# Kernel tuning notes

Hardware: AMD Instinct MI355X
Metric: run time of the kernel (lower is better)

## Reference

```python
import jax, jax.numpy as jnp
import numpy as np

R = 4                      # search_range
D = 2 * R + 1              # 9 -> 81 cost channels
FILTERS = [128, 128, 96, 64, 32, 2]


def mish(x):
    return x * jnp.tanh(jax.nn.softplus(x))


def sep_conv(x, dw, pw, b, act):
    # depthwise 3x3 (depth_multiplier=1), then pointwise 1x1, bias after pointwise
    y = jax.lax.conv_general_dilated(
        x, dw, window_strides=(1, 1), padding='SAME',
        dimension_numbers=('NHWC', 'HWIO', 'NHWC'),
        feature_group_count=x.shape[-1])
    y = jax.lax.conv_general_dilated(
        y, pw, window_strides=(1, 1), padding='SAME',
        dimension_numbers=('NHWC', 'HWIO', 'NHWC'))
    if b is not None:
        y = y + b
    return mish(y) if act else y


def cost_volume(prv, nxt):
    B, H, W, C = prv.shape
    pad = jnp.pad(nxt, ((0, 0), (R, R), (R, R), (0, 0)))
    # (2R+1)^2 shifted correlations, mean over channels (matches tf.reduce_mean axis=3)
    costs = [jnp.mean(prv * pad[:, i:i + H, j:j + W, :], axis=3)
             for i in range(D) for j in range(D)]
    return jnp.stack(costs, axis=3)  # [B,H,W,81]


def setup_inputs() -> dict:
    key = jax.random.key(0)
    ks = jax.random.split(key, 40)
    B, H, W, C = 8, 128, 128, 128
    inp = {
        'prv': jax.random.normal(ks[0], (B, H, W, C), jnp.float32),
        'nxt': jax.random.normal(ks[1], (B, H, W, C), jnp.float32),
    }
    in_ch = [D * D + 2 * C] + FILTERS[:-1]  # [337,128,128,96,64,32]
    ki = 2
    for i, (ci, f) in enumerate(zip(in_ch, FILTERS)):
        inp[f'dw{i}'] = jax.random.normal(ks[ki], (3, 3, 1, ci), jnp.float32) * 0.05; ki += 1
        inp[f'pw{i}'] = jax.random.normal(ks[ki], (1, 1, ci, f), jnp.float32) * 0.05; ki += 1
        if i < len(FILTERS) - 1:  # last layer: use_bias=False
            inp[f'b{i}'] = jnp.zeros((f,), jnp.float32)
    return inp


def reference(prv, nxt,
              dw0, pw0, b0, dw1, pw1, b1, dw2, pw2, b2,
              dw3, pw3, b3, dw4, pw4, b4, dw5, pw5):
    cost = cost_volume(prv, nxt)
    x = jnp.concatenate([cost, prv, nxt], axis=-1)
    x = sep_conv(x, dw0, pw0, b0, True)
    x = sep_conv(x, dw1, pw1, b1, True)
    x = sep_conv(x, dw2, pw2, b2, True)
    x = sep_conv(x, dw3, pw3, b3, True)
    x = sep_conv(x, dw4, pw4, b4, True)
    x = sep_conv(x, dw5, pw5, None, False)  # flow head: no bias, no activation
    return x
```

## Files before the change

kernel.cpp:

```cpp
#include <hip/hip_runtime.h>
#include <math.h>

#define BATCH 8
#define HH 128
#define WW 128
#define CC 128
#define RR 4
#define DDIM 9
#define NS 81
#define NSP 96
#define HWPIX (HH*WW)
#define DSLAB 1032

typedef short  short8  __attribute__((ext_vector_type(8)));
typedef float  f32x4   __attribute__((ext_vector_type(4)));

__device__ __forceinline__ short bf16h(float f){
    unsigned u = __float_as_uint(f);
    u += 0x7fffu + ((u >> 16) & 1u);
    return (short)(u >> 16);
}
__device__ __forceinline__ float bf16f(short s){
    return __uint_as_float(((unsigned)(unsigned short)s) << 16);
}
__device__ __forceinline__ float mish_f(float x){
    float xc = fminf(x, 30.f);
    float t = expf(xc);
    float u = t*t + 2.f*t;
    return x * (u / (u + 2.f));
}

__device__ __forceinline__ void gld16(float* lds, const float* g){
    __builtin_amdgcn_global_load_lds(
        (const __attribute__((address_space(1))) unsigned int*)g,
        (__attribute__((address_space(3))) unsigned int*)lds, 16, 0, 0);
}

__device__ __forceinline__ void lds_barrier(){
    __asm volatile("s_waitcnt lgkmcnt(0)\n\ts_barrier" ::: "memory");
}

__global__ void zero_k(float* p, int n){
    int i = blockIdx.x*256 + threadIdx.x;
    if(i < n) p[i] = 0.f;
}

__global__ __launch_bounds__(256,2) void cost_kernel(
    const float* __restrict__ prv, const float* __restrict__ nxt,
    const float* __restrict__ zb, float* __restrict__ cost)
{
    __shared__ float nx[2][2304*2];
    const int tid = threadIdx.x;
    const int tx = tid & 15, ty = tid >> 4;
    const int x0 = blockIdx.x*16, y0 = blockIdx.y*16, b = blockIdx.z;

    float acc[NS];
#pragma unroll
    for(int s=0;s<NS;s++) acc[s]=0.f;

    const float* prvp = prv + (((size_t)b*HH + (y0+ty))*WW + (x0+tx))*CC;
    const float* nxb  = nxt + (size_t)b*HH*WW*CC;

    auto stagec = [&](int c0, int pb){
        float* xp = &nx[pb][0];
#pragma unroll
        for(int it=0;it<5;it++){
            int e = it*256 + tid;
            if(e < 1152){
                int q = (e >= 576) ? 1 : 0;
                int p = e - q*576;
                int row = p/24, col = p - row*24;
                int hy = y0 - RR + row, hx = x0 - RR + col;
                bool ok = hy>=0 && hy<HH && hx>=0 && hx<WW;
                const float* gp = ok ? (nxb + ((size_t)hy*WW + hx)*CC + c0 + q*4)
                                     : zb;
                gld16(xp + e*4, gp);
            }
        }
    };

    float4 pAr = *(const float4*)(prvp);
    float4 pBr = *(const float4*)(prvp + 4);
    stagec(0, 0);
    int pb = 0;
    for(int c0=0;c0<CC;c0+=8){
        __syncthreads();
        float4 A = pAr, Bv = pBr;
        if(c0+8 < CC){
            pAr = *(const float4*)(prvp + c0 + 8);
            pBr = *(const float4*)(prvp + c0 + 12);
            stagec(c0+8, pb^1);
        }
        const float* xp = &nx[pb][0];
#pragma unroll
        for(int i=0;i<DDIM;i++){
            const float* rp = xp + (((ty+i)*24 + tx))*4;
#pragma unroll
            for(int j=0;j<DDIM;j++){
                float4 n0 = *(const float4*)(rp + j*4);
                float4 n1 = *(const float4*)(rp + j*4 + 2304);
                float s = acc[i*DDIM+j];
                s = fmaf(A.x,n0.x,s);  s = fmaf(A.y,n0.y,s);
                s = fmaf(A.z,n0.z,s);  s = fmaf(A.w,n0.w,s);
                s = fmaf(Bv.x,n1.x,s); s = fmaf(Bv.y,n1.y,s);
                s = fmaf(Bv.z,n1.z,s); s = fmaf(Bv.w,n1.w,s);
                acc[i*DDIM+j] = s;
            }
        }
        pb ^= 1;
    }
    float* op = cost + (((size_t)b*HH + (y0+ty))*WW + (x0+tx))*NSP;
#pragma unroll
    for(int g=0; g<NSP/4; g++){
        float4 v;
        int s = g*4;
        v.x = (s   < NS) ? acc[s  ]*(1.f/128.f) : 0.f;
        v.y = (s+1 < NS) ? acc[s+1]*(1.f/128.f) : 0.f;
        v.z = (s+2 < NS) ? acc[s+2]*(1.f/128.f) : 0.f;
        v.w = (s+3 < NS) ? acc[s+3]*(1.f/128.f) : 0.f;
        *(float4*)(op + s) = v;
    }
}

__global__ void prep_pw(const float* __restrict__ src, short* __restrict__ dh,
                        short* __restrict__ dl, int K, int N, int NP, int total,
                        int remap)
{
    int idx = blockIdx.x*256 + threadIdx.x;
    if(idx >= total) return;
    int j  = idx & 7;
    int n  = (idx>>3) % NP;
    int k8 = (idx>>3) / NP;
    int k  = k8*8 + j;
    if(remap) k = (k < 81) ? k : ((k < 96) ? -1 : k - 15);
    float v = (k>=0 && k<K && n<N) ? src[(size_t)k*N + n] : 0.f;
    short h = bf16h(v);
    dh[idx] = h;
    dl[idx] = bf16h(v - bf16f(h));
}

__global__ void prep_dw(const float* __restrict__ src, float* __restrict__ dst,
                        int K, int K0, int remap, int total)
{
    int idx = blockIdx.x*256 + threadIdx.x;
    if(idx >= total) return;
    int k = idx / K0, c = idx - k*K0;
    int cr = c;
    if(remap) cr = (c < 81) ? c : ((c < 96) ? -1 : c - 15);
    dst[idx] = (cr>=0 && cr<K) ? src[k*K + cr] : 0.f;
}

template<int CINR,int K0,int COUT,int NP,bool BIAS,bool ACT,bool CONCAT>
__global__ __launch_bounds__(256,2) void sep_mfma(
    const float* __restrict__ xin, const float* __restrict__ cost,
    const float* __restrict__ prv, const float* __restrict__ nxt,
    const float* __restrict__ dwp, const short* __restrict__ wh,
    const short* __restrict__ wl, const float* __restrict__ bias,
    const float* __restrict__ zb, float* __restrict__ out)
{
    constexpr int TN = NP/32;
    __shared__ float xs[2][180*36];
    __shared__ short dshh[4*DSLAB];
    __shared__ short dshl[4*DSLAB];
    __shared__ float dwls[2][9*32];

    const int tid = threadIdx.x;
    const int x0 = blockIdx.x*16, y0 = blockIdx.y*8, b = blockIdx.z;
    const int lane = tid & 63;
    const int wv   = tid >> 6;
    const int wm   = wv >> 1, wn = wv & 1;
    const int l15  = lane & 15, quad = lane >> 4;

    f32x4 acc[4][TN];
#pragma unroll
    for(int i=0;i<4;i++)
#pragma unroll
        for(int nt=0;nt<TN;nt++) acc[i][nt] = (f32x4){0.f,0.f,0.f,0.f};

    auto stage = [&](int c0, int pb){
        if(tid < 72)
            gld16(&dwls[pb][(tid>>3)*32 + (tid&7)*4],
                  dwp + (tid>>3)*K0 + c0 + (tid&7)*4);
        const float* src; int str, coff;
        if(CONCAT){
            if(c0 < 96)      { src = cost; str = NSP; coff = c0; }
            else if(c0 < 224){ src = prv;  str = 128; coff = c0-96; }
            else             { src = nxt;  str = 128; coff = c0-224; }
        } else { src = xin; str = CINR; coff = c0; }
        const float* sb = src + (size_t)b*HH*WW*str + coff;
        float* xp = &xs[pb][0];
#pragma unroll
        for(int it=0;it<7;it++){
            int e = it*256 + tid;
            if(e < 1620){
                int hp = e/9, q = e - hp*9;
                int hy = y0-1 + hp/18, hx = x0-1 + hp%18;
                bool ok = (q < 8) && hy>=0 && hy<HH && hx>=0 && hx<WW;
                const float* gp = ok ? (sb + ((size_t)hy*WW + hx)*str + q*4)
                                     : zb;
                gld16(xp + hp*36 + q*4, gp);
            }
        }
    };

    const int c4  = tid & 7;
    const int pxg = tid >> 3;
    const int dpy = pxg >> 2;
    const int dxb = (pxg & 3) * 4;

    stage(0, 0);
    int pb = 0;
    for(int c0=0;c0<K0;c0+=32){
        __syncthreads();
        const int k8 = (c0>>3) + quad;
        short8 Bh[TN], Bl[TN];
#pragma unroll
        for(int nt=0;nt<TN;nt++){
            int n = wn*(NP/2) + nt*16 + l15;
            size_t off = ((size_t)k8*NP + n)*8;
            Bh[nt] = *(const short8*)(wh + off);
            Bl[nt] = *(const short8*)(wl + off);
        }
        if(c0+32 < K0) stage(c0+32, pb^1);
        const float* xp = &xs[pb][0];
        const float* dwc = &dwls[pb][0];
        {
            float4 o[4];
#pragma unroll
            for(int dx=0;dx<4;dx++) o[dx] = make_float4(0.f,0.f,0.f,0.f);
#pragma unroll
            for(int kh=0;kh<3;kh++){
                float4 xw[6];
#pragma unroll
                for(int t=0;t<6;t++)
                    xw[t] = *(const float4*)&xp[((dpy+kh)*18 + dxb + t)*36 + c4*4];
#pragma unroll
                for(int kw=0;kw<3;kw++){
                    float4 w4 = *(const float4*)&dwc[(kh*3+kw)*32 + c4*4];
#pragma unroll
                    for(int dx=0;dx<4;dx++){
                        float4 xv = xw[kw+dx];
                        o[dx].x = fmaf(xv.x,w4.x,o[dx].x);
                        o[dx].y = fmaf(xv.y,w4.y,o[dx].y);
                        o[dx].z = fmaf(xv.z,w4.z,o[dx].z);
                        o[dx].w = fmaf(xv.w,w4.w,o[dx].w);
                    }
                }
            }
            const int wbase = (c4>>1)*DSLAB + (pxg*4)*8 + (c4&1)*4;
#pragma unroll
            for(int dx=0;dx<4;dx++){
                float4 s = o[dx];
                short h0=bf16h(s.x), h1=bf16h(s.y), h2=bf16h(s.z), h3=bf16h(s.w);
                short l0=bf16h(s.x-bf16f(h0)), l1=bf16h(s.y-bf16f(h1));
                short l2=bf16h(s.z-bf16f(h2)), l3=bf16h(s.w-bf16f(h3));
                *(short4*)&dshh[wbase + dx*8] = make_short4(h0,h1,h2,h3);
                *(short4*)&dshl[wbase + dx*8] = make_short4(l0,l1,l2,l3);
            }
        }
        lds_barrier();
#pragma unroll
        for(int i=0;i<4;i++){
            int ab = quad*DSLAB + (wm*64 + i*16 + l15)*8;
            short8 Ah = *(const short8*)&dshh[ab];
            short8 Al = *(const short8*)&dshl[ab];
#pragma unroll
            for(int nt=0;nt<TN;nt++){
                f32x4 c = acc[i][nt];
                c = __builtin_amdgcn_mfma_f32_16x16x32_bf16(Ah,Bh[nt],c,0,0,0);
                c = __builtin_amdgcn_mfma_f32_16x16x32_bf16(Al,Bh[nt],c,0,0,0);
                c = __builtin_amdgcn_mfma_f32_16x16x32_bf16(Ah,Bl[nt],c,0,0,0);
                acc[i][nt] = c;
            }
        }
        lds_barrier();
        pb ^= 1;
    }
#pragma unroll
    for(int i=0;i<4;i++){
        int pxb = wm*64 + i*16 + quad*4;
#pragma unroll
        for(int nt=0;nt<TN;nt++){
            int cout = wn*(NP/2) + nt*16 + l15;
            if(cout < COUT){
                float bv = BIAS ? bias[cout] : 0.f;
#pragma unroll
                for(int r=0;r<4;r++){
                    int p = pxb + r;
                    int y = y0 + (p>>4), x = x0 + (p&15);
                    float v = acc[i][nt][r] + bv;
                    if(ACT) v = mish_f(v);
                    out[(((size_t)b*HH + y)*WW + x)*COUT + cout] = v;
                }
            }
        }
    }
}

extern "C" void kernel_launch(void* const* d_in, const int* in_sizes, int n_in,
                              void* d_out, int out_size, void* d_ws, size_t ws_size,
                              hipStream_t stream)
{
    (void)in_sizes; (void)n_in; (void)out_size;
    const float* prv = (const float*)d_in[0];
    const float* nxt = (const float*)d_in[1];
    const float* dws[6] = {(const float*)d_in[2],(const float*)d_in[5],(const float*)d_in[8],
                           (const float*)d_in[11],(const float*)d_in[14],(const float*)d_in[17]};
    const float* pws[6] = {(const float*)d_in[3],(const float*)d_in[6],(const float*)d_in[9],
                           (const float*)d_in[12],(const float*)d_in[15],(const float*)d_in[18]};
    const float* b0  = (const float*)d_in[4];
    const float* b1  = (const float*)d_in[7];
    const float* b2  = (const float*)d_in[10];
    const float* b3  = (const float*)d_in[13];
    const float* b4  = (const float*)d_in[16];

    const int   Ks[6]   = {337,128,128, 96, 64, 32};
    const int   K0s[6]  = {352,128,128, 96, 64, 32};
    const int   Ns[6]   = {128,128, 96, 64, 32,  2};
    const int   NPs[6]  = {128,128, 96, 64, 32, 32};
    const int   rmp[6]  = {  1,  0,  0,  0,  0,  0};
    size_t offs[6]; size_t E = 0;
    for(int i=0;i<6;i++){ offs[i] = E; E += (size_t)K0s[i]*NPs[i]; }
    size_t dwoffs[6]; size_t Edw = 0;
    for(int i=0;i<6;i++){ dwoffs[i] = Edw; Edw += (size_t)9*K0s[i]; }

    short* Whs = (short*)d_ws;
    short* Wls = Whs + E;
    float* Dwp = (float*)((char*)d_ws + ((E*2*sizeof(short) + 255) & ~(size_t)255));
    float* Zb  = Dwp + Edw;
    size_t wbytes = (((char*)(Zb + 64) - (char*)d_ws) + 255) & ~(size_t)255;

    zero_k<<<1,64,0,stream>>>(Zb, 64);
    for(int i=0;i<6;i++){
        int total = K0s[i]*NPs[i];
        prep_pw<<<(total+255)/256,256,0,stream>>>(pws[i], Whs+offs[i], Wls+offs[i],
                                                  Ks[i], Ns[i], NPs[i], total, rmp[i]);
        int tdw = 9*K0s[i];
        prep_dw<<<(tdw+255)/256,256,0,stream>>>(dws[i], Dwp+dwoffs[i],
                                                Ks[i], K0s[i], rmp[i], tdw);
    }

    const size_t per_batch_floats = (size_t)HWPIX * (NSP + 128 + 128);
    size_t avail = (ws_size > wbytes) ? (ws_size - wbytes) : 0;
    int NB = (int)(avail / (per_batch_floats * sizeof(float)));
    if(NB > BATCH) NB = BATCH;
    if(NB < 1)     NB = 1;
    while(BATCH % NB) NB--;

    float* fbase = (float*)((char*)d_ws + wbytes);
    float* costb = fbase;
    float* bufA  = costb + (size_t)NB*HWPIX*NSP;
    float* bufB  = bufA  + (size_t)NB*HWPIX*128;

    for(int bb=0; bb<BATCH; bb+=NB){
        const float* prv_o = prv + (size_t)bb*HWPIX*CC;
        const float* nxt_o = nxt + (size_t)bb*HWPIX*CC;
        float*       out_o = (float*)d_out + (size_t)bb*HWPIX*2;
        dim3 gc(WW/16, HH/16, NB);
        dim3 gs(WW/16, HH/8,  NB);

        cost_kernel<<<gc,256,0,stream>>>(prv_o, nxt_o, Zb, costb);
        sep_mfma<337,352,128,128,true ,true ,true ><<<gs,256,0,stream>>>(nullptr, costb, prv_o, nxt_o, Dwp+dwoffs[0], Whs+offs[0], Wls+offs[0], b0, Zb, bufA);
        sep_mfma<128,128,128,128,true ,true ,false><<<gs,256,0,stream>>>(bufA, nullptr,nullptr,nullptr, Dwp+dwoffs[1], Whs+offs[1], Wls+offs[1], b1, Zb, bufB);
        sep_mfma<128,128, 96, 96,true ,true ,false><<<gs,256,0,stream>>>(bufB, nullptr,nullptr,nullptr, Dwp+dwoffs[2], Whs+offs[2], Wls+offs[2], b2, Zb, bufA);
        sep_mfma< 96, 96, 64, 64,true ,true ,false><<<gs,256,0,stream>>>(bufA, nullptr,nullptr,nullptr, Dwp+dwoffs[3], Whs+offs[3], Wls+offs[3], b3, Zb, bufB);
        sep_mfma< 64, 64, 32, 32,true ,true ,false><<<gs,256,0,stream>>>(bufB, nullptr,nullptr,nullptr, Dwp+dwoffs[4], Whs+offs[4], Wls+offs[4], b4, Zb, bufA);
        sep_mfma< 32, 32,  2, 32,false,false,false><<<gs,256,0,stream>>>(bufA, nullptr,nullptr,nullptr, Dwp+dwoffs[5], Whs+offs[5], Wls+offs[5], nullptr, Zb, out_o);
    }
}
```

Measured before the change: 576.9 us.

## Compute cost volume with split-bf16 MFMA instead of scalar FMAs

Replaces the scalar-FMA correlation kernel with an MFMA kernel. Each wave computes 16x16 pixel-by-shift tiles per row offset, using a hi/lo bf16 split (four MFMAs per tile) to keep roughly fp32 accuracy. Shifted nxt tiles are converted to bf16 hi/lo in LDS with register-prefetch double staging, and only the valid diagonal band of each tile is written out. This wastes part of each MFMA on shifts outside the band and adds conversion work in exchange for matrix-core throughput.

```diff
diff --git a/kernel.cpp b/kernel.cpp
--- a/kernel.cpp
+++ b/kernel.cpp
@@ -45,80 +45,135 @@
     if(i < n) p[i] = 0.f;
 }
 
-__global__ __launch_bounds__(256,2) void cost_kernel(
+__device__ __forceinline__ void cvt8(const float4& a, const float4& b,
+                                     short8& h, short8& l){
+    float v0=a.x,v1=a.y,v2=a.z,v3=a.w,v4=b.x,v5=b.y,v6=b.z,v7=b.w;
+    short h0=bf16h(v0),h1=bf16h(v1),h2=bf16h(v2),h3=bf16h(v3);
+    short h4=bf16h(v4),h5=bf16h(v5),h6=bf16h(v6),h7=bf16h(v7);
+    h[0]=h0;h[1]=h1;h[2]=h2;h[3]=h3;h[4]=h4;h[5]=h5;h[6]=h6;h[7]=h7;
+    l[0]=bf16h(v0-bf16f(h0)); l[1]=bf16h(v1-bf16f(h1));
+    l[2]=bf16h(v2-bf16f(h2)); l[3]=bf16h(v3-bf16f(h3));
+    l[4]=bf16h(v4-bf16f(h4)); l[5]=bf16h(v5-bf16f(h5));
+    l[6]=bf16h(v6-bf16f(h6)); l[7]=bf16h(v7-bf16f(h7));
+}
+
+__global__ __launch_bounds__(512,4) void cost_mfma(
     const float* __restrict__ prv, const float* __restrict__ nxt,
-    const float* __restrict__ zb, float* __restrict__ cost)
+    float* __restrict__ cost)
 {
-    __shared__ float nx[2][2304*2];
-    const int tid = threadIdx.x;
-    const int tx = tid & 15, ty = tid >> 4;
+    __shared__ short bhs[24*4*24*8];
+    __shared__ short bls[24*4*24*8];
+    const int tid  = threadIdx.x;
+    const int lane = tid & 63, wv = tid >> 6;
+    const int l15  = lane & 15, quad = lane >> 4;
     const int x0 = blockIdx.x*16, y0 = blockIdx.y*16, b = blockIdx.z;
-
-    float acc[NS];
-#pragma unroll
-    for(int s=0;s<NS;s++) acc[s]=0.f;
-
-    const float* prvp = prv + (((size_t)b*HH + (y0+ty))*WW + (x0+tx))*CC;
+    const int Y = wv*2;
+
+    const float* prvb = prv + (((size_t)b*HH + y0)*WW + x0)*CC;
     const float* nxb  = nxt + (size_t)b*HH*WW*CC;
 
-    auto stagec = [&](int c0, int pb){
-        float* xp = &nx[pb][0];
-#pragma unroll
-        for(int it=0;it<5;it++){
-            int e = it*256 + tid;
-            if(e < 1152){
-                int q = (e >= 576) ? 1 : 0;
-                int p = e - q*576;
-                int row = p/24, col = p - row*24;
-                int hy = y0 - RR + row, hx = x0 - RR + col;
-                bool ok = hy>=0 && hy<HH && hx>=0 && hx<WW;
-                const float* gp = ok ? (nxb + ((size_t)hy*WW + hx)*CC + c0 + q*4)
-                                     : zb;
-                gld16(xp + e*4, gp);
-            }
+    f32x4 acc[2][9][2];
+#pragma unroll
+    for(int yy=0;yy<2;yy++)
+#pragma unroll
+        for(int i=0;i<9;i++){
+            acc[yy][i][0] = (f32x4){0.f,0.f,0.f,0.f};
+            acc[yy][i][1] = (f32x4){0.f,0.f,0.f,0.f};
+        }
+
+    if(tid < 256){
+        float* zp = cost + (((size_t)b*HH + y0 + (tid>>4))*WW + x0 + (tid&15))*NSP;
+        zp[81]=0.f; zp[82]=0.f; zp[83]=0.f;
+        float4 z4 = make_float4(0.f,0.f,0.f,0.f);
+        *(float4*)(zp+84)=z4; *(float4*)(zp+88)=z4; *(float4*)(zp+92)=z4;
+    }
+
+    float4 sreg[9];
+    auto sload = [&](int kc){
+#pragma unroll
+        for(int s=0;s<9;s++){
+            int e = s*512 + tid;
+            int px = e >> 3, q = e & 7;
+            int r = px/24, c = px - r*24;
+            int hy = y0 - 4 + r, hx = x0 - 4 + c;
+            bool ok = hy>=0 && hy<HH && hx>=0 && hx<WW;
+            sreg[s] = ok ? *(const float4*)(nxb + ((size_t)hy*WW + hx)*CC + kc*32 + q*4)
+                         : make_float4(0.f,0.f,0.f,0.f);
         }
     };
-
-    float4 pAr = *(const float4*)(prvp);
-    float4 pBr = *(const float4*)(prvp + 4);
-    stagec(0, 0);
-    int pb = 0;
-    for(int c0=0;c0<CC;c0+=8){
+    sload(0);
+
+    for(int kc=0; kc<4; kc++){
         __syncthreads();
-        float4 A = pAr, Bv = pBr;
-        if(c0+8 < CC){
-            pAr = *(const float4*)(prvp + c0 + 8);
-            pBr = *(const float4*)(prvp + c0 + 12);
-            stagec(c0+8, pb^1);
-        }
-        const float* xp = &nx[pb][0];
-#pragma unroll
-        for(int i=0;i<DDIM;i++){
-            const float* rp = xp + (((ty+i)*24 + tx))*4;
-#pragma unroll
-            for(int j=0;j<DDIM;j++){
-                float4 n0 = *(const float4*)(rp + j*4);
-                float4 n1 = *(const float4*)(rp + j*4 + 2304);
-                float s = acc[i*DDIM+j];
-                s = fmaf(A.x,n0.x,s);  s = fmaf(A.y,n0.y,s);
-                s = fmaf(A.z,n0.z,s);  s = fmaf(A.w,n0.w,s);
-                s = fmaf(Bv.x,n1.x,s); s = fmaf(Bv.y,n1.y,s);
-                s = fmaf(Bv.z,n1.z,s); s = fmaf(Bv.w,n1.w,s);
-                acc[i*DDIM+j] = s;
-            }
-        }
-        pb ^= 1;
-    }
-    float* op = cost + (((size_t)b*HH + (y0+ty))*WW + (x0+tx))*NSP;
-#pragma unroll
-    for(int g=0; g<NSP/4; g++){
-        float4 v;
-        int s = g*4;
-        v.x = (s   < NS) ? acc[s  ]*(1.f/128.f) : 0.f;
-        v.y = (s+1 < NS) ? acc[s+1]*(1.f/128.f) : 0.f;
-        v.z = (s+2 < NS) ? acc[s+2]*(1.f/128.f) : 0.f;
-        v.w = (s+3 < NS) ? acc[s+3]*(1.f/128.f) : 0.f;
-        *(float4*)(op + s) = v;
+#pragma unroll
+        for(int s=0;s<9;s++){
+            int e = s*512 + tid;
+            int px = e >> 3, q = e & 7;
+            int r = px/24, c = px - r*24;
+            int base = ((r*4 + (q>>1))*24 + c)*8 + (q&1)*4;
+            float4 v = sreg[s];
+            short h0=bf16h(v.x), h1=bf16h(v.y), h2=bf16h(v.z), h3=bf16h(v.w);
+            *(short4*)&bhs[base] = make_short4(h0,h1,h2,h3);
+            *(short4*)&bls[base] = make_short4(bf16h(v.x-bf16f(h0)),
+                                               bf16h(v.y-bf16f(h1)),
+                                               bf16h(v.z-bf16f(h2)),
+                                               bf16h(v.w-bf16f(h3)));
+        }
+        if(kc < 3) sload(kc+1);
+        short8 Ah[2], Al[2];
+#pragma unroll
+        for(int yy=0; yy<2; yy++){
+            const float* ap = prvb + ((size_t)(Y+yy)*WW + l15)*CC + kc*32 + quad*8;
+            float4 f0v = *(const float4*)ap;
+            float4 f1v = *(const float4*)(ap+4);
+            cvt8(f0v, f1v, Ah[yy], Al[yy]);
+        }
+        lds_barrier();
+#pragma unroll
+        for(int rr=0; rr<10; rr++){
+            int r  = Y + rr;
+            int rb = (r*4 + quad)*24*8;
+            short8 Bh0 = *(const short8*)&bhs[rb + l15*8];
+            short8 Bl0 = *(const short8*)&bls[rb + l15*8];
+            short8 Bh1 = *(const short8*)&bhs[rb + (8+l15)*8];
+            short8 Bl1 = *(const short8*)&bls[rb + (8+l15)*8];
+#pragma unroll
+            for(int yy=0; yy<2; yy++){
+                int i = rr - yy;
+                if(i >= 0 && i <= 8){
+                    f32x4 c0 = acc[yy][i][0];
+                    c0 = __builtin_amdgcn_mfma_f32_16x16x32_bf16(Ah[yy],Bh0,c0,0,0,0);
+                    c0 = __builtin_amdgcn_mfma_f32_16x16x32_bf16(Al[yy],Bh0,c0,0,0,0);
+                    c0 = __builtin_amdgcn_mfma_f32_16x16x32_bf16(Ah[yy],Bl0,c0,0,0,0);
+                    c0 = __builtin_amdgcn_mfma_f32_16x16x32_bf16(Al[yy],Bl0,c0,0,0,0);
+                    acc[yy][i][0] = c0;
+                    f32x4 c1 = acc[yy][i][1];
+                    c1 = __builtin_amdgcn_mfma_f32_16x16x32_bf16(Ah[yy],Bh1,c1,0,0,0);
+                    c1 = __builtin_amdgcn_mfma_f32_16x16x32_bf16(Al[yy],Bh1,c1,0,0,0);
+                    c1 = __builtin_amdgcn_mfma_f32_16x16x32_bf16(Ah[yy],Bl1,c1,0,0,0);
+                    c1 = __builtin_amdgcn_mfma_f32_16x16x32_bf16(Al[yy],Bl1,c1,0,0,0);
+                    acc[yy][i][1] = c1;
+                }
+            }
+        }
+    }
+    const float sc = 1.f/128.f;
+#pragma unroll
+    for(int yy=0; yy<2; yy++){
+        float* orow = cost + (((size_t)b*HH + (y0+Y+yy))*WW + x0)*NSP;
+#pragma unroll
+        for(int i=0;i<9;i++){
+#pragma unroll
+            for(int rg=0; rg<4; rg++){
+                int m  = quad*4 + rg;
+                int j0 = l15 - m;
+                if(j0 >= 0 && j0 <= 8)
+                    orow[(size_t)m*NSP + i*9 + j0] = acc[yy][i][0][rg]*sc;
+                int j1 = 8 + l15 - m;
+                if(l15 >= 8 && j1 <= 8)
+                    orow[(size_t)m*NSP + i*9 + j1] = acc[yy][i][1][rg]*sc;
+            }
+        }
     }
 }
 
@@ -359,7 +414,7 @@
         dim3 gc(WW/16, HH/16, NB);
         dim3 gs(WW/16, HH/8,  NB);
 
-        cost_kernel<<<gc,256,0,stream>>>(prv_o, nxt_o, Zb, costb);
+        cost_mfma<<<gc,512,0,stream>>>(prv_o, nxt_o, costb);
         sep_mfma<337,352,128,128,true ,true ,true ><<<gs,256,0,stream>>>(nullptr, costb, prv_o, nxt_o, Dwp+dwoffs[0], Whs+offs[0], Wls+offs[0], b0, Zb, bufA);
         sep_mfma<128,128,128,128,true ,true ,false><<<gs,256,0,stream>>>(bufA, nullptr,nullptr,nullptr, Dwp+dwoffs[1], Whs+offs[1], Wls+offs[1], b1, Zb, bufB);
         sep_mfma<128,128, 96, 96,true ,true ,false><<<gs,256,0,stream>>>(bufB, nullptr,nullptr,nullptr, Dwp+dwoffs[2], Whs+offs[2], Wls+offs[2], b2, Zb, bufA);
```

After: 772.6 us. 33.9% more time.
